# Performance work log

Measured on AMD Instinct MI355X. Metric: run time of the kernel, lower is better.

## Reference

```python
import jax, jax.numpy as jnp
import numpy as np

N_ATOMS = 100000
M_NBR = 12
ATOM_F = 64
NBR_F = 41
BN_EPS = 1e-5


def setup_inputs() -> dict:
    key = jax.random.key(0)
    ks = jax.random.split(key, 6)
    atom_in_fea = jax.random.normal(ks[0], (N_ATOMS, ATOM_F), dtype=jnp.float32)
    nbr_fea = jax.random.normal(ks[1], (N_ATOMS, M_NBR, NBR_F), dtype=jnp.float32)
    nbr_fea_idx = jax.random.randint(ks[2], (N_ATOMS, M_NBR), 0, N_ATOMS)
    in_dim = 2 * ATOM_F + NBR_F  # 169
    out_dim = 2 * ATOM_F  # 128
    # torch nn.Linear init scale
    bound = 1.0 / np.sqrt(in_dim)
    fc_w = jax.random.uniform(ks[3], (out_dim, in_dim), minval=-bound, maxval=bound, dtype=jnp.float32)
    fc_b = jax.random.uniform(ks[4], (out_dim,), minval=-bound, maxval=bound, dtype=jnp.float32)
    return {
        "atom_in_fea": atom_in_fea,
        "nbr_fea": nbr_fea,
        "nbr_fea_idx": nbr_fea_idx,
        "fc_w": fc_w,
        "fc_b": fc_b,
        "bn1_gamma": jnp.ones((out_dim,), jnp.float32),
        "bn1_beta": jnp.zeros((out_dim,), jnp.float32),
        "bn2_gamma": jnp.ones((ATOM_F,), jnp.float32),
        "bn2_beta": jnp.zeros((ATOM_F,), jnp.float32),
    }


def _batchnorm(x, gamma, beta):
    # training-mode BN (torch default): biased batch statistics over axis 0
    mean = x.mean(axis=0)
    var = x.var(axis=0)
    return (x - mean) * jax.lax.rsqrt(var + BN_EPS) * gamma + beta


def reference(atom_in_fea, nbr_fea, nbr_fea_idx, fc_w, fc_b,
              bn1_gamma, bn1_beta, bn2_gamma, bn2_beta):
    N, M = nbr_fea_idx.shape
    F = atom_in_fea.shape[1]
    atom_nbr_fea = atom_in_fea[nbr_fea_idx]                      # [N, M, F] gather
    self_fea = jnp.broadcast_to(atom_in_fea[:, None, :], (N, M, F))
    total_nbr_fea = jnp.concatenate([self_fea, atom_nbr_fea, nbr_fea], axis=2)  # [N, M, 2F+E]
    gated = jnp.einsum('nmi,oi->nmo', total_nbr_fea, fc_w) + fc_b               # [N, M, 2F]
    gated = _batchnorm(gated.reshape(-1, 2 * F), bn1_gamma, bn1_beta).reshape(N, M, 2 * F)
    nbr_filter = jax.nn.sigmoid(gated[..., :F])
    nbr_core = jax.nn.softplus(gated[..., F:])
    nbr_sumed = jnp.sum(nbr_filter * nbr_core, axis=1)           # [N, F]
    nbr_sumed = _batchnorm(nbr_sumed, bn2_gamma, bn2_beta)
    return jax.nn.softplus(atom_in_fea + nbr_sumed)
```

## Files before the change

kernel.cpp:

```cpp
#include <hip/hip_runtime.h>
#include <stdint.h>

typedef __attribute__((ext_vector_type(8))) short bf16x8;
typedef __attribute__((ext_vector_type(4))) float f32x4;

static constexpr int MNBR   = 12;
static constexpr int AF     = 64;
static constexpr int EF     = 41;
static constexpr int IN_DIM = 2 * AF + EF;
static constexpr float BN_EPS = 1e-5f;

static constexpr int EW_ROW_U16 = 132;

__device__ __forceinline__ float bfu(uint16_t u) {
    return __uint_as_float(((uint32_t)u) << 16);
}
__device__ __forceinline__ uint16_t f2bfbits(float f) {
    uint32_t x = __float_as_uint(f);
    uint32_t r = x + 0x7fffu + ((x >> 16) & 1u);
    return (uint16_t)(r >> 16);
}
__device__ __forceinline__ float softplusf(float x) {
    return fmaxf(x, 0.f) + __logf(1.0f + __expf(-fabsf(x)));
}

__global__ __launch_bounds__(256) void k_prep(
    const float* __restrict__ fc_w, uint16_t* __restrict__ wp_proj,
    uint16_t* __restrict__ wp_edge)
{
    int e = blockIdx.x * 256 + threadIdx.x;
    if (e < 16384) {
        int j = e & 7, lane = (e >> 3) & 63, s = (e >> 9) & 1, t = e >> 10;
        int n = lane & 15, q = lane >> 4;
        int k = s * 32 + q * 8 + j;
        int c = t * 16 + n;
        float v = (c < 128) ? fc_w[c * IN_DIM + k]
                            : fc_w[(c - 128) * IN_DIM + 64 + k];
        wp_proj[e] = f2bfbits(v);
    } else if (e < 24576) {
        int e2 = e - 16384;
        int j = e2 & 7, lane = (e2 >> 3) & 63, s = (e2 >> 9) & 1, t = e2 >> 10;
        int n = lane & 15, q = lane >> 4;
        int k = s * 32 + q * 8 + j;
        int o = t * 16 + n;
        wp_edge[e2] = (k < EF) ? f2bfbits(fc_w[o * IN_DIM + 2 * AF + k])
                               : (uint16_t)0;
    }
}

__global__ __launch_bounds__(256) void k_proj(
    const float* __restrict__ atom_in, const uint16_t* __restrict__ wp_proj,
    const float* __restrict__ fc_b, uint16_t* __restrict__ P, int N)
{
    const int lane = threadIdx.x & 63;
    const int w    = __builtin_amdgcn_readfirstlane((int)(threadIdx.x >> 6));
    const int a0   = blockIdx.x * 64 + w * 16;
    const int mrow = lane & 15, q = lane >> 4;
    const int arow = a0 + mrow;

    bf16x8 A0 = {}, A1 = {};
    if (arow < N) {
        const float* pa = atom_in + (size_t)arow * AF;
#pragma unroll
        for (int j = 0; j < 8; ++j) {
            A0[j] = (short)f2bfbits(pa[q * 8 + j]);
            A1[j] = (short)f2bfbits(pa[32 + q * 8 + j]);
        }
    }

    const bf16x8* wp = (const bf16x8*)wp_proj;
#pragma unroll
    for (int t = 0; t < 16; ++t) {
        f32x4 acc = {0.f, 0.f, 0.f, 0.f};
        bf16x8 b0 = wp[(t * 2 + 0) * 64 + lane];
        bf16x8 b1 = wp[(t * 2 + 1) * 64 + lane];
        acc = __builtin_amdgcn_mfma_f32_16x16x32_bf16(A0, b0, acc, 0, 0, 0);
        acc = __builtin_amdgcn_mfma_f32_16x16x32_bf16(A1, b1, acc, 0, 0, 0);
        const int c = t * 16 + (lane & 15);
        const float bias = (c < 128) ? fc_b[c] : 0.f;
#pragma unroll
        for (int r = 0; r < 4; ++r) {
            const int row = q * 4 + r;
            const int atom = a0 + row;
            if (atom < N) P[(size_t)atom * 256 + c] = f2bfbits(acc[r] + bias);
        }
    }
}

template <int MODE>
__global__ __launch_bounds__(256) void k_conv(
    const uint16_t* __restrict__ P, const float* __restrict__ nbr,
    const int* __restrict__ idx, const uint16_t* __restrict__ wp_edge,
    const float* __restrict__ bn1coef, float* __restrict__ partial,
    float* __restrict__ nsum, int N)
{
    __shared__ uint16_t ew16[4][16 * EW_ROW_U16];
    __shared__ float red[4][256];

    const int lane = threadIdx.x & 63;
    const int w    = __builtin_amdgcn_readfirstlane((int)(threadIdx.x >> 6));
    const int col  = lane & 15, q = lane >> 4;
    const int o    = lane;

    const bf16x8* wpv = (const bf16x8*)wp_edge;
    bf16x8 B[8][2];
#pragma unroll
    for (int t = 0; t < 8; ++t) {
#pragma unroll
        for (int s = 0; s < 2; ++s) B[t][s] = wpv[(t * 2 + s) * 64 + lane];
    }

    const int rbase = blockIdx.x * 384 + w * 96;
    const int nbase = rbase / 12;

    float s1f = 0.f, h1f = 0.f, s1c = 0.f, h1c = 0.f;
    if (MODE == 1) {
        s1f = bn1coef[o];       h1f = bn1coef[128 + o];
        s1c = bn1coef[64 + o];  h1c = bn1coef[192 + o];
    }

    float sA = 0.f, qA = 0.f, sB = 0.f, qB = 0.f;
    float accm = 0.f, psf = 0.f, psc = 0.f;
    uint16_t* myew = ew16[w];

#pragma unroll
    for (int mt = 0; mt < 6; ++mt) {
        const int rs = rbase + mt * 16;
        const float* er = nbr + (size_t)(rs + col) * EF;
        bf16x8 A0, A1 = {};
#pragma unroll
        for (int j = 0; j < 8; ++j) A0[j] = (short)f2bfbits(er[q * 8 + j]);
        if (q == 0) {
#pragma unroll
            for (int j = 0; j < 8; ++j) A1[j] = (short)f2bfbits(er[32 + j]);
        } else if (q == 1) {
            A1[0] = (short)f2bfbits(er[40]);
        }
        f32x4 acc[8];
#pragma unroll
        for (int t = 0; t < 8; ++t) {
            f32x4 a = {0.f, 0.f, 0.f, 0.f};
            a = __builtin_amdgcn_mfma_f32_16x16x32_bf16(A0, B[t][0], a, 0, 0, 0);
            a = __builtin_amdgcn_mfma_f32_16x16x32_bf16(A1, B[t][1], a, 0, 0, 0);
            acc[t] = a;
        }
#pragma unroll
        for (int t = 0; t < 8; ++t) {
            const int ch  = t * 16 + col;
            const int pos = (ch < 64) ? (ch * 2) : ((ch - 64) * 2 + 1);
#pragma unroll
            for (int r = 0; r < 4; ++r) {
                const int row = q * 4 + r;
                myew[row * EW_ROW_U16 + pos] = f2bfbits(acc[t][r]);
            }
        }
        __syncthreads();
#pragma unroll
        for (int i = 0; i < 16; ++i) {
            const int g = mt * 16 + i;
            const int m = g % 12;
            const int n = nbase + g / 12;
            if (m == 0) {
                psf  = bfu(P[(size_t)n * 256 + o]);
                psc  = bfu(P[(size_t)n * 256 + 64 + o]);
                accm = 0.f;
            }
            const int r = rs + i;
            const int j = __builtin_amdgcn_readfirstlane(idx[r]);
            uint32_t pr;
            __builtin_memcpy(&pr, &myew[i * EW_ROW_U16 + 2 * o], 4);
            const float ewf = __uint_as_float(pr << 16);
            const float ewc = __uint_as_float(pr & 0xffff0000u);
            const float pnf = bfu(P[(size_t)j * 256 + 128 + o]);
            const float pnc = bfu(P[(size_t)j * 256 + 192 + o]);
            const float gf = ewf + psf + pnf;
            const float gc = ewc + psc + pnc;
            if (MODE == 0) {
                sA += gf; qA = fmaf(gf, gf, qA);
                sB += gc; qB = fmaf(gc, gc, qB);
            } else {
                const float xf = fmaf(gf, s1f, h1f);
                const float xc = fmaf(gc, s1c, h1c);
                const float filt = 1.0f / (1.0f + __expf(-xf));
                accm = fmaf(filt, softplusf(xc), accm);
            }
            if (m == 11 && MODE == 1) {
                nsum[(size_t)n * AF + o] = accm;
                sB += accm; qB = fmaf(accm, accm, qB);
            }
        }
        __syncthreads();
    }

    if (MODE == 0) {
        red[w][0 * 64 + lane] = sA;
        red[w][1 * 64 + lane] = qA;
        red[w][2 * 64 + lane] = sB;
        red[w][3 * 64 + lane] = qB;
        __syncthreads();
        const int s = threadIdx.x;
        const int oc = (s & 127) >> 1;
        const int v  = (s >> 7) * 2 + (s & 1);
        const int mp = v * 64 + oc;
        partial[(size_t)blockIdx.x * 256 + s] =
            red[0][mp] + red[1][mp] + red[2][mp] + red[3][mp];
    } else {
        red[w][0 * 64 + lane] = sB;
        red[w][1 * 64 + lane] = qB;
        __syncthreads();
        const int s = threadIdx.x;
        if (s < 128) {
            const int oc = s >> 1;
            const int v  = s & 1;
            const int mp = v * 64 + oc;
            partial[(size_t)blockIdx.x * 128 + s] =
                red[0][mp] + red[1][mp] + red[2][mp] + red[3][mp];
        }
    }
}

__global__ __launch_bounds__(256) void k_bn_fin(
    const float* __restrict__ partial, const float* __restrict__ gamma,
    const float* __restrict__ beta, float* __restrict__ coef,
    int nch, int NB, float invR)
{
    const int c = blockIdx.x;
    const int tid = threadIdx.x;
    float s = 0.f, qq = 0.f;
    for (int i = tid; i < NB; i += 256) {
        const float* pp = partial + (size_t)i * (2 * nch) + 2 * c;
        s += pp[0]; qq += pp[1];
    }
    __shared__ float ls[256], lq[256];
    ls[tid] = s; lq[tid] = qq;
    __syncthreads();
    for (int off = 128; off > 0; off >>= 1) {
        if (tid < off) { ls[tid] += ls[tid + off]; lq[tid] += lq[tid + off]; }
        __syncthreads();
    }
    if (tid == 0) {
        float mean = ls[0] * invR;
        float var  = fmaxf(lq[0] * invR - mean * mean, 0.f);
        float sc = gamma[c] * rsqrtf(var + BN_EPS);
        coef[c]       = sc;
        coef[nch + c] = beta[c] - mean * sc;
    }
}

__global__ __launch_bounds__(256) void k_final(
    const float* __restrict__ atom_in, const float* __restrict__ nsum,
    const float* __restrict__ bn2, float* __restrict__ out, int total)
{
    int i = blockIdx.x * 256 + threadIdx.x;
    if (i >= total) return;
    int f = i & (AF - 1);
    float v = fmaf(nsum[i], bn2[f], bn2[AF + f]);
    float x = atom_in[i] + v;
    out[i] = softplusf(x);
}

extern "C" void kernel_launch(void* const* d_in, const int* in_sizes, int n_in,
                              void* d_out, int out_size, void* d_ws, size_t ws_size,
                              hipStream_t stream)
{
    const float* atom_in = (const float*)d_in[0];
    const float* nbr_fea = (const float*)d_in[1];
    const int*   nbr_idx = (const int*)d_in[2];
    const float* fc_w    = (const float*)d_in[3];
    const float* fc_b    = (const float*)d_in[4];
    const float* g1      = (const float*)d_in[5];
    const float* b1      = (const float*)d_in[6];
    const float* g2      = (const float*)d_in[7];
    const float* b2      = (const float*)d_in[8];
    float* out = (float*)d_out;

    const int N = in_sizes[0] / AF;
    const int conv_blocks = N / 32;
    const int NB = conv_blocks;

    char* ws = (char*)d_ws;
    size_t off = 0;
    uint16_t* wp_proj = (uint16_t*)(ws + off); off += 16384 * 2;
    uint16_t* wp_edge = (uint16_t*)(ws + off); off += 8192 * 2;
    uint16_t* P  = (uint16_t*)(ws + off); off += (size_t)N * 256 * 2;
    float* bn1  = (float*)(ws + off);  off += 256 * 4;
    float* bn2c = (float*)(ws + off);  off += 128 * 4;
    off = (off + 511) & ~(size_t)511;
    float* nsum = (float*)(ws + off);
    float* p1   = nsum;
    off += (size_t)N * AF * 4;
    float* p2   = (float*)(ws + off);  off += (size_t)NB * 128 * 4;

    k_prep<<<96, 256, 0, stream>>>(fc_w, wp_proj, wp_edge);
    k_proj<<<(N + 63) / 64, 256, 0, stream>>>(atom_in, wp_proj, fc_b, P, N);
    k_conv<0><<<conv_blocks, 256, 0, stream>>>(P, nbr_fea, nbr_idx, wp_edge,
                                               nullptr, p1, nullptr, N);
    k_bn_fin<<<128, 256, 0, stream>>>(p1, g1, b1, bn1, 128, NB,
                                      1.0f / (float)(N * MNBR));
    k_conv<1><<<conv_blocks, 256, 0, stream>>>(P, nbr_fea, nbr_idx, wp_edge,
                                               bn1, p2, nsum, N);
    k_bn_fin<<<64, 256, 0, stream>>>(p2, g2, b2, bn2c, 64, NB, 1.0f / (float)N);

    const int total = N * AF;
    k_final<<<(total + 255) / 256, 256, 0, stream>>>(atom_in, nsum, bn2c, out,
                                                     total);
}
```

Measured before the change: 740.4 us.

## Interleave projection outputs into paired buffers and prefetch gathers in conv

The projection output is split into a self buffer and a neighbor buffer, with the filter and core channels interleaved so each lane fetches one 32-bit word per gather instead of two 16-bit loads. The conv kernel preloads the neighbor indices into registers and issues all 16 neighbor gathers of a tile up front. It also double-buffers the raw edge-feature loads for the next tile, stages the edge weights in shared memory instead of registers, and sets launch bounds to target three blocks per CU. The goal is to hide gather latency and cut load instruction count, at the cost of more shared memory and register pressure.

```diff
diff --git a/kernel.cpp b/kernel.cpp
--- a/kernel.cpp
+++ b/kernel.cpp
@@ -50,7 +50,8 @@
 
 __global__ __launch_bounds__(256) void k_proj(
     const float* __restrict__ atom_in, const uint16_t* __restrict__ wp_proj,
-    const float* __restrict__ fc_b, uint16_t* __restrict__ P, int N)
+    const float* __restrict__ fc_b, uint16_t* __restrict__ Ps,
+    uint16_t* __restrict__ Pn, int N)
 {
     const int lane = threadIdx.x & 63;
     const int w    = __builtin_amdgcn_readfirstlane((int)(threadIdx.x >> 6));
@@ -82,36 +83,53 @@
         for (int r = 0; r < 4; ++r) {
             const int row = q * 4 + r;
             const int atom = a0 + row;
-            if (atom < N) P[(size_t)atom * 256 + c] = f2bfbits(acc[r] + bias);
+            if (atom < N) {
+                const uint16_t v = f2bfbits(acc[r] + bias);
+                const size_t base = (size_t)atom * 128;
+                if (c < 64)       Ps[base + 2 * c] = v;
+                else if (c < 128) Ps[base + 2 * (c - 64) + 1] = v;
+                else if (c < 192) Pn[base + 2 * (c - 128)] = v;
+                else              Pn[base + 2 * (c - 192) + 1] = v;
+            }
         }
     }
 }
 
 template <int MODE>
-__global__ __launch_bounds__(256) void k_conv(
-    const uint16_t* __restrict__ P, const float* __restrict__ nbr,
-    const int* __restrict__ idx, const uint16_t* __restrict__ wp_edge,
-    const float* __restrict__ bn1coef, float* __restrict__ partial,
-    float* __restrict__ nsum, int N)
+__global__ __launch_bounds__(256, 3) void k_conv(
+    const uint32_t* __restrict__ Ps32, const uint32_t* __restrict__ Pn32,
+    const float* __restrict__ nbr, const int* __restrict__ idx,
+    const uint16_t* __restrict__ wp_edge, const float* __restrict__ bn1coef,
+    float* __restrict__ partial, float* __restrict__ nsum, int N)
 {
     __shared__ uint16_t ew16[4][16 * EW_ROW_U16];
     __shared__ float red[4][256];
-
-    const int lane = threadIdx.x & 63;
-    const int w    = __builtin_amdgcn_readfirstlane((int)(threadIdx.x >> 6));
+    __shared__ uint16_t bsh[8192];
+
+    const int tid  = threadIdx.x;
+    const int lane = tid & 63;
+    const int w    = __builtin_amdgcn_readfirstlane((int)(tid >> 6));
     const int col  = lane & 15, q = lane >> 4;
     const int o    = lane;
-
-    const bf16x8* wpv = (const bf16x8*)wp_edge;
-    bf16x8 B[8][2];
-#pragma unroll
-    for (int t = 0; t < 8; ++t) {
-#pragma unroll
-        for (int s = 0; s < 2; ++s) B[t][s] = wpv[(t * 2 + s) * 64 + lane];
-    }
+    (void)N;
 
     const int rbase = blockIdx.x * 384 + w * 96;
     const int nbase = rbase / 12;
+
+    int idxA = idx[rbase + lane];
+    int idxB = 0;
+    if (lane < 32) idxB = idx[rbase + 64 + lane];
+
+    uint32_t psv[8];
+#pragma unroll
+    for (int a = 0; a < 8; ++a) psv[a] = Ps32[(size_t)(nbase + a) * 64 + o];
+
+    {
+        const uint4* s4 = (const uint4*)wp_edge;
+        uint4* d4 = (uint4*)bsh;
+#pragma unroll
+        for (int k = 0; k < 4; ++k) d4[k * 256 + tid] = s4[k * 256 + tid];
+    }
 
     float s1f = 0.f, h1f = 0.f, s1c = 0.f, h1c = 0.f;
     if (MODE == 1) {
@@ -122,28 +140,70 @@
     float sA = 0.f, qA = 0.f, sB = 0.f, qB = 0.f;
     float accm = 0.f, psf = 0.f, psc = 0.f;
     uint16_t* myew = ew16[w];
+    const bf16x8* bvs = (const bf16x8*)bsh;
+
+    f32x4 r0[2], r1[2], rc0[2], rc1[2];
+    float re[2];
+
+    auto load_raw = [&](int mt, int buf) {
+        const float* er = nbr + (size_t)(rbase + mt * 16 + col) * EF;
+        __builtin_memcpy(&r0[buf], er + q * 8, 16);
+        __builtin_memcpy(&r1[buf], er + q * 8 + 4, 16);
+        rc0[buf] = f32x4{0.f, 0.f, 0.f, 0.f};
+        rc1[buf] = f32x4{0.f, 0.f, 0.f, 0.f};
+        re[buf] = 0.f;
+        if (q == 0) {
+            __builtin_memcpy(&rc0[buf], er + 32, 16);
+            __builtin_memcpy(&rc1[buf], er + 36, 16);
+        } else if (q == 1) {
+            re[buf] = er[40];
+        }
+    };
+
+    load_raw(0, 0);
+    __syncthreads();
+
+    uint32_t pnv[16];
 
 #pragma unroll
     for (int mt = 0; mt < 6; ++mt) {
-        const int rs = rbase + mt * 16;
-        const float* er = nbr + (size_t)(rs + col) * EF;
+        const int cur = mt & 1, nxt = cur ^ 1;
+
+#pragma unroll
+        for (int i = 0; i < 16; ++i) {
+            const int g = mt * 16 + i;
+            const int j = (g < 64) ? __builtin_amdgcn_readlane(idxA, g)
+                                   : __builtin_amdgcn_readlane(idxB, g - 64);
+            pnv[i] = Pn32[(size_t)j * 64 + o];
+        }
+
         bf16x8 A0, A1 = {};
 #pragma unroll
-        for (int j = 0; j < 8; ++j) A0[j] = (short)f2bfbits(er[q * 8 + j]);
+        for (int j = 0; j < 4; ++j) {
+            A0[j]     = (short)f2bfbits(r0[cur][j]);
+            A0[4 + j] = (short)f2bfbits(r1[cur][j]);
+        }
         if (q == 0) {
 #pragma unroll
-            for (int j = 0; j < 8; ++j) A1[j] = (short)f2bfbits(er[32 + j]);
+            for (int j = 0; j < 4; ++j) {
+                A1[j]     = (short)f2bfbits(rc0[cur][j]);
+                A1[4 + j] = (short)f2bfbits(rc1[cur][j]);
+            }
         } else if (q == 1) {
-            A1[0] = (short)f2bfbits(er[40]);
-        }
+            A1[0] = (short)f2bfbits(re[cur]);
+        }
+
         f32x4 acc[8];
 #pragma unroll
         for (int t = 0; t < 8; ++t) {
+            bf16x8 b0 = bvs[(t * 2 + 0) * 64 + lane];
+            bf16x8 b1 = bvs[(t * 2 + 1) * 64 + lane];
             f32x4 a = {0.f, 0.f, 0.f, 0.f};
-            a = __builtin_amdgcn_mfma_f32_16x16x32_bf16(A0, B[t][0], a, 0, 0, 0);
-            a = __builtin_amdgcn_mfma_f32_16x16x32_bf16(A1, B[t][1], a, 0, 0, 0);
+            a = __builtin_amdgcn_mfma_f32_16x16x32_bf16(A0, b0, a, 0, 0, 0);
+            a = __builtin_amdgcn_mfma_f32_16x16x32_bf16(A1, b1, a, 0, 0, 0);
             acc[t] = a;
         }
+
 #pragma unroll
         for (int t = 0; t < 8; ++t) {
             const int ch  = t * 16 + col;
@@ -154,25 +214,27 @@
                 myew[row * EW_ROW_U16 + pos] = f2bfbits(acc[t][r]);
             }
         }
-        __syncthreads();
+
+        if (mt < 5) load_raw(mt + 1, nxt);
+
+        __syncthreads();
+
 #pragma unroll
         for (int i = 0; i < 16; ++i) {
             const int g = mt * 16 + i;
             const int m = g % 12;
-            const int n = nbase + g / 12;
             if (m == 0) {
-                psf  = bfu(P[(size_t)n * 256 + o]);
-                psc  = bfu(P[(size_t)n * 256 + 64 + o]);
+                const uint32_t pp = psv[g / 12];
+                psf  = __uint_as_float(pp << 16);
+                psc  = __uint_as_float(pp & 0xffff0000u);
                 accm = 0.f;
             }
-            const int r = rs + i;
-            const int j = __builtin_amdgcn_readfirstlane(idx[r]);
             uint32_t pr;
             __builtin_memcpy(&pr, &myew[i * EW_ROW_U16 + 2 * o], 4);
             const float ewf = __uint_as_float(pr << 16);
             const float ewc = __uint_as_float(pr & 0xffff0000u);
-            const float pnf = bfu(P[(size_t)j * 256 + 128 + o]);
-            const float pnc = bfu(P[(size_t)j * 256 + 192 + o]);
+            const float pnf = __uint_as_float(pnv[i] << 16);
+            const float pnc = __uint_as_float(pnv[i] & 0xffff0000u);
             const float gf = ewf + psf + pnf;
             const float gc = ewc + psc + pnc;
             if (MODE == 0) {
@@ -183,10 +245,11 @@
                 const float xc = fmaf(gc, s1c, h1c);
                 const float filt = 1.0f / (1.0f + __expf(-xf));
                 accm = fmaf(filt, softplusf(xc), accm);
-            }
-            if (m == 11 && MODE == 1) {
-                nsum[(size_t)n * AF + o] = accm;
-                sB += accm; qB = fmaf(accm, accm, qB);
+                if (m == 11) {
+                    const int n = nbase + g / 12;
+                    nsum[(size_t)n * AF + o] = accm;
+                    sB += accm; qB = fmaf(accm, accm, qB);
+                }
             }
         }
         __syncthreads();
@@ -282,7 +345,8 @@
     size_t off = 0;
     uint16_t* wp_proj = (uint16_t*)(ws + off); off += 16384 * 2;
     uint16_t* wp_edge = (uint16_t*)(ws + off); off += 8192 * 2;
-    uint16_t* P  = (uint16_t*)(ws + off); off += (size_t)N * 256 * 2;
+    uint16_t* Ps = (uint16_t*)(ws + off); off += (size_t)N * 128 * 2;
+    uint16_t* Pn = (uint16_t*)(ws + off); off += (size_t)N * 128 * 2;
     float* bn1  = (float*)(ws + off);  off += 256 * 4;
     float* bn2c = (float*)(ws + off);  off += 128 * 4;
     off = (off + 511) & ~(size_t)511;
@@ -292,12 +356,16 @@
     float* p2   = (float*)(ws + off);  off += (size_t)NB * 128 * 4;
 
     k_prep<<<96, 256, 0, stream>>>(fc_w, wp_proj, wp_edge);
-    k_proj<<<(N + 63) / 64, 256, 0, stream>>>(atom_in, wp_proj, fc_b, P, N);
-    k_conv<0><<<conv_blocks, 256, 0, stream>>>(P, nbr_fea, nbr_idx, wp_edge,
+    k_proj<<<(N + 63) / 64, 256, 0, stream>>>(atom_in, wp_proj, fc_b, Ps, Pn, N);
+    k_conv<0><<<conv_blocks, 256, 0, stream>>>((const uint32_t*)Ps,
+                                               (const uint32_t*)Pn,
+                                               nbr_fea, nbr_idx, wp_edge,
                                                nullptr, p1, nullptr, N);
     k_bn_fin<<<128, 256, 0, stream>>>(p1, g1, b1, bn1, 128, NB,
                                       1.0f / (float)(N * MNBR));
-    k_conv<1><<<conv_blocks, 256, 0, stream>>>(P, nbr_fea, nbr_idx, wp_edge,
+    k_conv<1><<<conv_blocks, 256, 0, stream>>>((const uint32_t*)Ps,
+                                               (const uint32_t*)Pn,
+                                               nbr_fea, nbr_idx, wp_edge,
                                                bn1, p2, nsum, N);
     k_bn_fin<<<64, 256, 0, stream>>>(p2, g2, b2, bn2c, 64, NB, 1.0f / (float)N);
 
```

Measured after the change: 791.3 us. 6.9% more time.
